# Performance work log

Hardware: AMD Instinct MI355X
Metric: run time of the kernel (lower is better)

The kernel has to match this reference:

```python
import jax, jax.numpy as jnp
import numpy as np

B, S, E = 2, 2048, 4096
H, KV, D = 32, 8, 128  # heads, kv heads, head_dim
ROPE_BASE = 500000.0


def setup_inputs() -> dict:
    key = jax.random.key(0)
    ks = jax.random.split(key, 5)
    scale = 0.02
    return {
        "x": jax.random.normal(ks[0], (B, S, E), dtype=jnp.float32),
        "wq": jax.random.normal(ks[1], (E, E), dtype=jnp.float32) * scale,
        "wk": jax.random.normal(ks[2], (KV * D, E), dtype=jnp.float32) * scale,
        "wv": jax.random.normal(ks[3], (KV * D, E), dtype=jnp.float32) * scale,
        "wo": jax.random.normal(ks[4], (E, E), dtype=jnp.float32) * scale,
        "input_pos": jnp.arange(S, dtype=jnp.int64 if jax.config.jax_enable_x64 else jnp.int32),
    }


def _rope(xh, input_pos):
    # xh: [B, H, S, D]; standard llama rotate-half RoPE
    half = D // 2
    inv_freq = 1.0 / (ROPE_BASE ** (jnp.arange(0, half, dtype=jnp.float32) / half))
    ang = input_pos.astype(jnp.float32)[:, None] * inv_freq[None, :]  # [S, half]
    cos, sin = jnp.cos(ang), jnp.sin(ang)
    x1, x2 = xh[..., :half], xh[..., half:]
    return jnp.concatenate([x1 * cos - x2 * sin, x2 * cos + x1 * sin], axis=-1)


def reference(x, wq, wk, wv, wo, input_pos):
    bsz, seq_len, _ = x.shape
    q = (x @ wq.T).reshape(bsz, seq_len, H, D).transpose(0, 2, 1, 3)    # [B,H,S,D]
    k = (x @ wk.T).reshape(bsz, seq_len, KV, D).transpose(0, 2, 1, 3)   # [B,KV,S,D]
    v = (x @ wv.T).reshape(bsz, seq_len, KV, D).transpose(0, 2, 1, 3)
    # repeat_kv: B (H R) S D with R = H // KV
    rep = H // KV
    k = jnp.repeat(k, rep, axis=1)
    v = jnp.repeat(v, rep, axis=1)
    q = _rope(q, input_pos)
    k = _rope(k, input_pos)
    # causal SDPA
    scores = jnp.einsum("bhqd,bhkd->bhqk", q, k) / jnp.sqrt(jnp.float32(D))
    causal = jnp.tril(jnp.ones((seq_len, seq_len), dtype=bool))
    scores = jnp.where(causal, scores, jnp.finfo(scores.dtype).min)
    probs = jax.nn.softmax(scores, axis=-1)
    out = jnp.einsum("bhqk,bhkd->bhqd", probs, v)                       # [B,H,S,D]
    out = out.transpose(0, 2, 1, 3).reshape(bsz, seq_len, E)
    return out @ wo.T
```

## Files before the change

### kernel.cpp

```cpp
#include <hip/hip_runtime.h>

#define B_ 2
#define S_ 2048
#define E_ 4096
#define H_ 32
#define KV_ 8
#define D_ 128

typedef __bf16 v8bf __attribute__((ext_vector_type(8)));
typedef __bf16 v4bf __attribute__((ext_vector_type(4)));
typedef float  v4f  __attribute__((ext_vector_type(4)));

static __device__ __forceinline__ v4f mfma16(v8bf a, v8bf b, v4f c) {
    return __builtin_amdgcn_mfma_f32_16x16x32_bf16(a, b, c, 0, 0, 0);
}

static __device__ __forceinline__ void load_lds16(const void* g, void* l) {
    __builtin_amdgcn_global_load_lds(
        (const __attribute__((address_space(1))) void*)g,
        (__attribute__((address_space(3))) void*)l, 16, 0, 0);
}

__global__ __launch_bounds__(256) void cast_f32_to_bf16(
        const float4* __restrict__ in, v4bf* __restrict__ out, int n4) {
    int i = blockIdx.x * blockDim.x + threadIdx.x;
    if (i >= n4) return;
    float4 v = in[i];
    v4bf o;
    o[0] = (__bf16)v.x; o[1] = (__bf16)v.y; o[2] = (__bf16)v.z; o[3] = (__bf16)v.w;
    out[i] = o;
}

__global__ __launch_bounds__(256) void rope_inplace(
        __bf16* __restrict__ qk, const int* __restrict__ pos, int nh,
        int rowstride, float outscale) {
    int idx = blockIdx.x * blockDim.x + threadIdx.x;
    int d = idx & 63;
    int t = idx >> 6;
    int h = t % nh;
    int bs = t / nh;
    if (bs >= B_ * S_) return;
    int s = bs & (S_ - 1);
    float p = (float)pos[s];
    float inv = expf(-(float)d * (1.0f / 64.0f) * 13.122363377404329f);
    float ang = p * inv;
    float c = cosf(ang), sn = sinf(ang);
    size_t off = (size_t)bs * rowstride + (size_t)h * D_;
    float x1 = (float)qk[off + d];
    float x2 = (float)qk[off + d + 64];
    qk[off + d]      = (__bf16)((x1 * c - x2 * sn) * outscale);
    qk[off + d + 64] = (__bf16)((x2 * c + x1 * sn) * outscale);
}

template <int EPI>
__global__ __launch_bounds__(512, 2) void gemm_bt(
        const __bf16* __restrict__ A, const __bf16* __restrict__ Bm,
        void* __restrict__ Cv, void* __restrict__ Cv2, int M, int N, int K) {
    __shared__ __bf16 As[2][256 * 64];
    __shared__ __bf16 Bs[2][256 * 64];
    const int tid  = threadIdx.x;
    const int wave = tid >> 6;
    const int lane = tid & 63;
    const int l15  = lane & 15;
    const int quad = lane >> 4;

    const int nbx = N >> 8;
    const int nwg = (int)gridDim.x;
    const int swz = ((int)blockIdx.x & 7) * (nwg >> 3) + ((int)blockIdx.x >> 3);
    const int bm  = (swz / nbx) * 256;
    const int bn  = (swz % nbx) * 256;

    const int wr = wave >> 2;
    const int wc = wave & 3;

    v4f acc[8][4] = {};

    const int srow = wave * 8 + (lane >> 3);
    const int scc  = (lane & 7) ^ ((lane >> 3) & 7);

    auto stage = [&](int t, int buf) {
        const size_t k0 = (size_t)t * 64;
#pragma unroll
        for (int g = 0; g < 4; ++g) {
            load_lds16(A + (size_t)(bm + g * 64 + srow) * K + k0 + scc * 8,
                       (char*)&As[buf][0] + (size_t)g * 8192 + (size_t)wave * 1024);
            load_lds16(Bm + (size_t)(bn + g * 64 + srow) * K + k0 + scc * 8,
                       (char*)&Bs[buf][0] + (size_t)g * 8192 + (size_t)wave * 1024);
        }
    };

    stage(0, 0);

    const int nt = K >> 6;
    for (int t = 0; t < nt; ++t) {
        const int cur = t & 1;
        if (t + 1 < nt) {
            stage(t + 1, cur ^ 1);
            asm volatile("s_waitcnt vmcnt(8)" ::: "memory");
        } else {
            asm volatile("s_waitcnt vmcnt(0)" ::: "memory");
        }
        __builtin_amdgcn_s_barrier();
        __builtin_amdgcn_sched_barrier(0);

        const __bf16* Asc = &As[cur][0];
        const __bf16* Bsc = &Bs[cur][0];
        v8bf a[4][2], b[2][2];

        auto rdA = [&](int mh) {
#pragma unroll
            for (int i = 0; i < 4; ++i)
#pragma unroll
                for (int kk = 0; kk < 2; ++kk)
                    a[i][kk] = *(const v8bf*)&Asc[
                        (wr * 128 + mh * 64 + i * 16 + l15) * 64 +
                        (((kk * 4 + quad) ^ (l15 & 7)) * 8)];
        };
        auto rdB = [&](int nh) {
#pragma unroll
            for (int j = 0; j < 2; ++j)
#pragma unroll
                for (int kk = 0; kk < 2; ++kk)
                    b[j][kk] = *(const v8bf*)&Bsc[
                        (wc * 64 + nh * 32 + j * 16 + l15) * 64 +
                        (((kk * 4 + quad) ^ (l15 & 7)) * 8)];
        };
        auto domfma = [&](int mh, int nh) {
            __builtin_amdgcn_s_setprio(1);
#pragma unroll
            for (int kk = 0; kk < 2; ++kk)
#pragma unroll
                for (int i = 0; i < 4; ++i)
#pragma unroll
                    for (int j = 0; j < 2; ++j)
                        acc[mh * 4 + i][nh * 2 + j] =
                            mfma16(a[i][kk], b[j][kk], acc[mh * 4 + i][nh * 2 + j]);
            __builtin_amdgcn_s_setprio(0);
        };

        rdA(0); rdB(0);
        __builtin_amdgcn_s_barrier();
        domfma(0, 0);
        __builtin_amdgcn_s_barrier();
        __builtin_amdgcn_sched_barrier(0);
        rdB(1);
        __builtin_amdgcn_s_barrier();
        domfma(0, 1);
        __builtin_amdgcn_s_barrier();
        __builtin_amdgcn_sched_barrier(0);
        rdA(1);
        __builtin_amdgcn_s_barrier();
        domfma(1, 1);
        __builtin_amdgcn_s_barrier();
        __builtin_amdgcn_sched_barrier(0);
        rdB(0);
        __builtin_amdgcn_s_barrier();
        domfma(1, 0);
        __builtin_amdgcn_s_barrier();
        __builtin_amdgcn_sched_barrier(0);
    }

#pragma unroll
    for (int mi = 0; mi < 8; ++mi) {
#pragma unroll
        for (int nj = 0; nj < 4; ++nj) {
#pragma unroll
            for (int r = 0; r < 4; ++r) {
                int row = bm + wr * 128 + mi * 16 + quad * 4 + r;
                int col = bn + wc * 64 + nj * 16 + l15;
                float val = acc[mi][nj][r];
                if (EPI == 0) {
                    ((float*)Cv)[(size_t)row * N + col] = val;
                } else if (EPI == 1) {
                    ((__bf16*)Cv)[(size_t)row * N + col] = (__bf16)val;
                } else {
                    if (col < 1024) {
                        ((__bf16*)Cv)[(size_t)row * 1024 + col] = (__bf16)val;
                    } else {
                        int cc = col - 1024;
                        int b  = row >> 11, s = row & (S_ - 1);
                        int kv = cc >> 7,  d = cc & (D_ - 1);
                        ((__bf16*)Cv2)[((size_t)((b * KV_ + kv) * D_ + d)) * S_ + s] = (__bf16)val;
                    }
                }
            }
        }
    }
}

__global__ __launch_bounds__(256, 2) void attn_fused(
        const __bf16* __restrict__ q, const __bf16* __restrict__ k,
        const __bf16* __restrict__ vt, __bf16* __restrict__ attn) {
    __shared__ __bf16 Ks[2][64 * 128];
    __shared__ __bf16 Vs[2][128 * 64];
    __shared__ __bf16 P[4][16 * 64];
    const int wave = threadIdx.x >> 6;
    const int lane = threadIdx.x & 63;

    const int wgid = blockIdx.x;
    const int xcd  = wgid & 7;
    const int slot = wgid >> 3;
    const int bh   = xcd * 8 + (slot >> 5);
    const int qblk = 31 - (slot & 31);
    const int b = bh >> 5;
    const int h = bh & 31;
    const int kvh = h >> 2;
    const int q0 = qblk * 64 + wave * 16;
    const int l15  = lane & 15;
    const int quad = lane >> 4;

    const __bf16* qbase = q  + (size_t)(b * S_) * E_ + (size_t)h * D_;
    const __bf16* kbase = k  + (size_t)(b * S_) * (KV_ * D_) + (size_t)kvh * D_;
    const __bf16* vbase = vt + (size_t)((b * KV_ + kvh) * D_) * S_;
    __bf16* Pw = &P[wave][0];

    const int krow_l = lane >> 4;
    const int kcc    = lane & 15;
    const int vrow_l = lane >> 3;
    const int vcc    = lane & 7;

    auto stageK = [&](int t, int buf) {
#pragma unroll
        for (int i = 0; i < 4; ++i) {
            int g = wave * 4 + i;
            int row = g * 4 + krow_l;
            int scc = kcc ^ (row & 15);
            load_lds16(kbase + (size_t)(t * 64 + row) * (KV_ * D_) + scc * 8,
                       (char*)&Ks[buf][0] + (size_t)g * 1024);
        }
    };
    auto stageV = [&](int t, int buf) {
#pragma unroll
        for (int i = 0; i < 4; ++i) {
            int g = wave * 4 + i;
            int row = g * 8 + vrow_l;
            int scc = vcc ^ (row & 7);
            load_lds16(vbase + (size_t)row * S_ + t * 64 + scc * 8,
                       (char*)&Vs[buf][0] + (size_t)g * 1024);
        }
    };

    stageK(0, 0);
    stageV(0, 0);

    v8bf aq[4];
#pragma unroll
    for (int kc = 0; kc < 4; ++kc)
        aq[kc] = *(const v8bf*)(qbase + (size_t)(q0 + l15) * E_ + kc * 32 + quad * 8);

    v4f o[8] = {};
    float m_i = -INFINITY, l_i = 0.f;

    const int ntiles = qblk + 1;

    for (int t = 0; t < ntiles; ++t) {
        const int cur = t & 1;
        if (t + 1 < ntiles) {
            stageK(t + 1, cur ^ 1);
            stageV(t + 1, cur ^ 1);
            asm volatile("s_waitcnt vmcnt(8)" ::: "memory");
        } else {
            asm volatile("s_waitcnt vmcnt(0)" ::: "memory");
        }
        __builtin_amdgcn_s_barrier();
        __builtin_amdgcn_sched_barrier(0);

        const int n0 = t * 64;
        const __bf16* Ksc = &Ks[cur][0];
        const __bf16* Vsc = &Vs[cur][0];

        v4f s[4] = {};
        __builtin_amdgcn_s_setprio(1);
#pragma unroll
        for (int kc = 0; kc < 4; ++kc) {
            v8bf kf[4];
#pragma unroll
            for (int j = 0; j < 4; ++j)
                kf[j] = *(const v8bf*)&Ksc[(j * 16 + l15) * 128 +
                                           (((kc * 4 + quad) ^ l15) * 8)];
#pragma unroll
            for (int j = 0; j < 4; ++j)
                s[j] = mfma16(kf[j], aq[kc], s[j]);
        }
        __builtin_amdgcn_s_setprio(0);

        float e[4][4];
        if (n0 + 63 > q0) {
#pragma unroll
            for (int j = 0; j < 4; ++j)
#pragma unroll
                for (int r = 0; r < 4; ++r) {
                    float v = s[j][r];
                    if (n0 + j * 16 + quad * 4 + r > q0 + l15) v = -INFINITY;
                    e[j][r] = v;
                }
        } else {
#pragma unroll
            for (int j = 0; j < 4; ++j)
#pragma unroll
                for (int r = 0; r < 4; ++r)
                    e[j][r] = s[j][r];
        }

        float mloc = e[0][0];
#pragma unroll
        for (int j = 0; j < 4; ++j)
#pragma unroll
            for (int r = 0; r < 4; ++r)
                mloc = fmaxf(mloc, e[j][r]);
        mloc = fmaxf(mloc, __shfl_xor(mloc, 16, 64));
        mloc = fmaxf(mloc, __shfl_xor(mloc, 32, 64));

        if (!__all(mloc - m_i <= 8.0f)) {
            float mnew = fmaxf(m_i, mloc);
            float alpha = __expf(m_i - mnew);
            m_i = mnew;
            l_i *= alpha;
            float af[4];
#pragma unroll
            for (int r = 0; r < 4; ++r)
                af[r] = __shfl(alpha, quad * 4 + r, 16);
#pragma unroll
            for (int c = 0; c < 8; ++c)
#pragma unroll
                for (int r = 0; r < 4; ++r)
                    o[c][r] *= af[r];
        }

        float psum = 0.f;
#pragma unroll
        for (int j = 0; j < 4; ++j)
#pragma unroll
            for (int r = 0; r < 4; ++r) {
                e[j][r] = __expf(e[j][r] - m_i);
                psum += e[j][r];
            }
        psum += __shfl_xor(psum, 16, 64);
        psum += __shfl_xor(psum, 32, 64);
        l_i += psum;

#pragma unroll
        for (int j = 0; j < 4; ++j) {
            v4bf pk;
#pragma unroll
            for (int r = 0; r < 4; ++r) pk[r] = (__bf16)e[j][r];
            int cl = j * 2 + (quad >> 1);
            *(v4bf*)&Pw[l15 * 64 + ((cl ^ (l15 & 7)) << 3) + ((quad & 1) << 2)] = pk;
        }

        v8bf ap0 = *(const v8bf*)&Pw[l15 * 64 + ((quad ^ (l15 & 7)) << 3)];
        v8bf ap1 = *(const v8bf*)&Pw[l15 * 64 + (((4 + quad) ^ (l15 & 7)) << 3)];

        __builtin_amdgcn_s_setprio(1);
#pragma unroll
        for (int c = 0; c < 8; ++c) {
            v8bf v0 = *(const v8bf*)&Vsc[(c * 16 + l15) * 64 +
                                         ((quad ^ (l15 & 7)) * 8)];
            v8bf v1 = *(const v8bf*)&Vsc[(c * 16 + l15) * 64 +
                                         (((4 + quad) ^ (l15 & 7)) * 8)];
            o[c] = mfma16(ap0, v0, o[c]);
            o[c] = mfma16(ap1, v1, o[c]);
        }
        __builtin_amdgcn_s_setprio(0);

        __builtin_amdgcn_sched_barrier(0);
        asm volatile("s_waitcnt lgkmcnt(0)" ::: "memory");
        __builtin_amdgcn_s_barrier();
        __builtin_amdgcn_sched_barrier(0);
    }

    float linv = 1.0f / l_i;
    float lr[4];
#pragma unroll
    for (int r = 0; r < 4; ++r)
        lr[r] = __shfl(linv, quad * 4 + r, 16);
    __bf16* obase = attn + (size_t)(b * S_) * E_ + (size_t)h * D_;
#pragma unroll
    for (int c = 0; c < 8; ++c)
#pragma unroll
        for (int r = 0; r < 4; ++r)
            obase[(size_t)(q0 + quad * 4 + r) * E_ + c * 16 + l15] =
                (__bf16)(o[c][r] * lr[r]);
}

extern "C" void kernel_launch(void* const* d_in, const int* in_sizes, int n_in,
                              void* d_out, int out_size, void* d_ws, size_t ws_size,
                              hipStream_t stream) {
    (void)in_sizes; (void)n_in; (void)out_size; (void)ws_size;
    const float* x  = (const float*)d_in[0];
    const float* wq = (const float*)d_in[1];
    const float* wk = (const float*)d_in[2];
    const float* wv = (const float*)d_in[3];
    const float* wo = (const float*)d_in[4];
    const int*   pos = (const int*)d_in[5];
    float* out = (float*)d_out;

    char* ws = (char*)d_ws;
    size_t off = 0;
    auto alloc = [&](size_t bytes) {
        char* p = ws + off;
        off += (bytes + 255) & ~(size_t)255;
        return p;
    };
    __bf16* xb   = (__bf16*)alloc((size_t)B_ * S_ * E_ * 2);
    __bf16* wqb  = (__bf16*)alloc((size_t)E_ * E_ * 2);
    __bf16* wkvb = (__bf16*)alloc((size_t)2 * KV_ * D_ * E_ * 2);
    __bf16* wob  = (__bf16*)alloc((size_t)E_ * E_ * 2);
    __bf16* qb   = (__bf16*)alloc((size_t)B_ * S_ * E_ * 2);
    __bf16* kb   = (__bf16*)alloc((size_t)B_ * S_ * KV_ * D_ * 2);
    __bf16* vt   = (__bf16*)alloc((size_t)B_ * KV_ * D_ * S_ * 2);
    __bf16* at   = (__bf16*)alloc((size_t)B_ * S_ * E_ * 2);

    auto cast = [&](const float* in, __bf16* ob, size_t n) {
        int n4 = (int)(n / 4);
        cast_f32_to_bf16<<<(n4 + 255) / 256, 256, 0, stream>>>(
            (const float4*)in, (v4bf*)ob, n4);
    };
    cast(x,  xb,  (size_t)B_ * S_ * E_);
    cast(wq, wqb, (size_t)E_ * E_);
    cast(wk, wkvb, (size_t)KV_ * D_ * E_);
    cast(wv, wkvb + (size_t)KV_ * D_ * E_, (size_t)KV_ * D_ * E_);
    cast(wo, wob, (size_t)E_ * E_);

    const int M = B_ * S_;
    const int nwg_e = (E_ / 256) * (M / 256);
    const int nwg_kv = (2 * KV_ * D_ / 256) * (M / 256);
    gemm_bt<1><<<dim3(nwg_e), 512, 0, stream>>>(
        xb, wqb, qb, nullptr, M, E_, E_);
    gemm_bt<2><<<dim3(nwg_kv), 512, 0, stream>>>(
        xb, wkvb, kb, vt, M, 2 * KV_ * D_, E_);

    rope_inplace<<<(B_ * S_ * H_ * 64 + 255) / 256, 256, 0, stream>>>(
        qb, pos, H_, E_, 0.08838834764831845f);
    rope_inplace<<<(B_ * S_ * KV_ * 64 + 255) / 256, 256, 0, stream>>>(
        kb, pos, KV_, KV_ * D_, 1.0f);

    attn_fused<<<dim3(B_ * H_ * (S_ / 64)), 256, 0, stream>>>(qb, kb, vt, at);

    gemm_bt<0><<<dim3(nwg_e), 512, 0, stream>>>(
        at, wob, out, nullptr, M, E_, E_);
}
```

Measured before the change: 889.1 us.

## Remove per-quadrant barriers in GEMM inner loop and keep both B halves in registers

Replaces the four read/barrier/MFMA phases per K-tile with one larger phase. Both B halves are held in registers (b0, b1), so the second rdB(0) reload is gone. The intra-tile s_barrier calls that kept waves in lockstep are removed, leaving one lgkmcnt wait and one barrier at the end of each tile. This cuts synchronisation and redundant LDS reads, but raises register pressure and gives up the explicit wave interleaving that let MFMA overlap LDS traffic across waves.

```diff
diff --git a/kernel.cpp b/kernel.cpp
--- a/kernel.cpp
+++ b/kernel.cpp
@@ -105,57 +105,71 @@
 
         const __bf16* Asc = &As[cur][0];
         const __bf16* Bsc = &Bs[cur][0];
-        v8bf a[4][2], b[2][2];
-
-        auto rdA = [&](int mh) {
+        v8bf a[4][2], b0[2][2], b1[2][2];
+
+#pragma unroll
+        for (int i = 0; i < 4; ++i)
+#pragma unroll
+            for (int kk = 0; kk < 2; ++kk)
+                a[i][kk] = *(const v8bf*)&Asc[
+                    (wr * 128 + i * 16 + l15) * 64 +
+                    (((kk * 4 + quad) ^ (l15 & 7)) * 8)];
+#pragma unroll
+        for (int j = 0; j < 2; ++j)
+#pragma unroll
+            for (int kk = 0; kk < 2; ++kk) {
+                b0[j][kk] = *(const v8bf*)&Bsc[
+                    (wc * 64 + j * 16 + l15) * 64 +
+                    (((kk * 4 + quad) ^ (l15 & 7)) * 8)];
+                b1[j][kk] = *(const v8bf*)&Bsc[
+                    (wc * 64 + 32 + j * 16 + l15) * 64 +
+                    (((kk * 4 + quad) ^ (l15 & 7)) * 8)];
+            }
+
+        __builtin_amdgcn_s_setprio(1);
+#pragma unroll
+        for (int kk = 0; kk < 2; ++kk)
 #pragma unroll
             for (int i = 0; i < 4; ++i)
 #pragma unroll
-                for (int kk = 0; kk < 2; ++kk)
-                    a[i][kk] = *(const v8bf*)&Asc[
-                        (wr * 128 + mh * 64 + i * 16 + l15) * 64 +
-                        (((kk * 4 + quad) ^ (l15 & 7)) * 8)];
-        };
-        auto rdB = [&](int nh) {
-#pragma unroll
-            for (int j = 0; j < 2; ++j)
-#pragma unroll
-                for (int kk = 0; kk < 2; ++kk)
-                    b[j][kk] = *(const v8bf*)&Bsc[
-                        (wc * 64 + nh * 32 + j * 16 + l15) * 64 +
-                        (((kk * 4 + quad) ^ (l15 & 7)) * 8)];
-        };
-        auto domfma = [&](int mh, int nh) {
-            __builtin_amdgcn_s_setprio(1);
+                for (int j = 0; j < 2; ++j)
+                    acc[i][j] = mfma16(a[i][kk], b0[j][kk], acc[i][j]);
+#pragma unroll
+        for (int kk = 0; kk < 2; ++kk)
+#pragma unroll
+            for (int i = 0; i < 4; ++i)
+#pragma unroll
+                for (int j = 0; j < 2; ++j)
+                    acc[i][2 + j] = mfma16(a[i][kk], b1[j][kk], acc[i][2 + j]);
+        __builtin_amdgcn_s_setprio(0);
+
+#pragma unroll
+        for (int i = 0; i < 4; ++i)
 #pragma unroll
             for (int kk = 0; kk < 2; ++kk)
-#pragma unroll
-                for (int i = 0; i < 4; ++i)
-#pragma unroll
-                    for (int j = 0; j < 2; ++j)
-                        acc[mh * 4 + i][nh * 2 + j] =
-                            mfma16(a[i][kk], b[j][kk], acc[mh * 4 + i][nh * 2 + j]);
-            __builtin_amdgcn_s_setprio(0);
-        };
-
-        rdA(0); rdB(0);
-        __builtin_amdgcn_s_barrier();
-        domfma(0, 0);
-        __builtin_amdgcn_s_barrier();
-        __builtin_amdgcn_sched_barrier(0);
-        rdB(1);
-        __builtin_amdgcn_s_barrier();
-        domfma(0, 1);
-        __builtin_amdgcn_s_barrier();
-        __builtin_amdgcn_sched_barrier(0);
-        rdA(1);
-        __builtin_amdgcn_s_barrier();
-        domfma(1, 1);
-        __builtin_amdgcn_s_barrier();
-        __builtin_amdgcn_sched_barrier(0);
-        rdB(0);
-        __builtin_amdgcn_s_barrier();
-        domfma(1, 0);
+                a[i][kk] = *(const v8bf*)&Asc[
+                    (wr * 128 + 64 + i * 16 + l15) * 64 +
+                    (((kk * 4 + quad) ^ (l15 & 7)) * 8)];
+
+        __builtin_amdgcn_s_setprio(1);
+#pragma unroll
+        for (int kk = 0; kk < 2; ++kk)
+#pragma unroll
+            for (int i = 0; i < 4; ++i)
+#pragma unroll
+                for (int j = 0; j < 2; ++j)
+                    acc[4 + i][2 + j] = mfma16(a[i][kk], b1[j][kk], acc[4 + i][2 + j]);
+#pragma unroll
+        for (int kk = 0; kk < 2; ++kk)
+#pragma unroll
+            for (int i = 0; i < 4; ++i)
+#pragma unroll
+                for (int j = 0; j < 2; ++j)
+                    acc[4 + i][j] = mfma16(a[i][kk], b0[j][kk], acc[4 + i][j]);
+        __builtin_amdgcn_s_setprio(0);
+
+        __builtin_amdgcn_sched_barrier(0);
+        asm volatile("s_waitcnt lgkmcnt(0)" ::: "memory");
         __builtin_amdgcn_s_barrier();
         __builtin_amdgcn_sched_barrier(0);
     }
```

After: 816.1 us. 8.2% less time.

## Fuse Q/KV projection GEMMs and pipeline quarter-tile LDS loads

Applied to the files above, without the earlier changes.

Merges the Q and KV projection GEMMs into one 384-workgroup launch, so the small KV GEMM no longer runs alone with poor occupancy and one launch is removed. The GEMM main loop now splits the LDS tile into four quarter buffers (A-top, B-left, B-right, A-bottom). It issues each quarter's next-k load right after that quarter is read, overlapping global-to-LDS transfers with MFMA phases. This adds finer vmcnt/barrier bookkeeping and more barriers per iteration, which could cost synchronization overhead.

```diff
diff --git a/kernel.cpp b/kernel.cpp
--- a/kernel.cpp
+++ b/kernel.cpp
@@ -52,17 +52,191 @@
     qk[off + d + 64] = (__bf16)((x2 * c + x1 * sn) * outscale);
 }
 
-template <int EPI>
-__global__ __launch_bounds__(512, 2) void gemm_bt(
-        const __bf16* __restrict__ A, const __bf16* __restrict__ Bm,
-        void* __restrict__ Cv, void* __restrict__ Cv2, int M, int N, int K) {
-    __shared__ __bf16 As[2][256 * 64];
-    __shared__ __bf16 Bs[2][256 * 64];
+#define GEMM_BODY(A_, Bm_, bm_, bn_, K_, H_ls, acc_)                           \
+    {                                                                          \
+        const int srow8 = tid >> 3;                                            \
+        const int scc   = (tid & 7) ^ (srow8 & 7);                             \
+        auto stageHT = [&](int t, int hh) {                                    \
+            char* dbase = (char*)&H_ls[t & 1][hh][0] + (size_t)wave * 1024;    \
+            const size_t kof = (size_t)t * 64 + scc * 8;                       \
+            if (hh == 0 || hh == 3) {                                          \
+                const int mh = (hh == 3);                                      \
+                _Pragma("unroll")                                              \
+                for (int g = 0; g < 2; ++g) {                                  \
+                    int row = bm_ + g * 128 + mh * 64 + srow8;                 \
+                    load_lds16(A_ + (size_t)row * K_ + kof, dbase + g * 8192); \
+                }                                                              \
+            } else {                                                           \
+                const int nh = (hh == 2);                                      \
+                _Pragma("unroll")                                              \
+                for (int g = 0; g < 2; ++g) {                                  \
+                    int sc  = g * 64 + srow8;                                  \
+                    int col = bn_ + (sc >> 5) * 64 + nh * 32 + (sc & 31);      \
+                    load_lds16(Bm_ + (size_t)col * K_ + kof, dbase + g * 8192);\
+                }                                                              \
+            }                                                                  \
+        };                                                                     \
+        stageHT(0, 0); stageHT(0, 1); stageHT(0, 2); stageHT(0, 3);            \
+        asm volatile("s_waitcnt vmcnt(4)" ::: "memory");                       \
+        __builtin_amdgcn_s_barrier();                                          \
+        const int nt = K_ >> 6;                                                \
+        for (int t = 0; t < nt; ++t) {                                         \
+            const int cur = t & 1;                                             \
+            const bool more = (t + 1 < nt);                                    \
+            const __bf16* A0p = &H_ls[cur][0][0];                              \
+            const __bf16* B0p = &H_ls[cur][1][0];                              \
+            const __bf16* B1p = &H_ls[cur][2][0];                              \
+            const __bf16* A1p = &H_ls[cur][3][0];                              \
+            v8bf a[4][2], b0[2][2], b1[2][2];                                  \
+            _Pragma("unroll")                                                  \
+            for (int i = 0; i < 4; ++i)                                        \
+                _Pragma("unroll")                                              \
+                for (int kk = 0; kk < 2; ++kk)                                 \
+                    a[i][kk] = *(const v8bf*)&A0p[(wr * 64 + i * 16 + l15) * 64\
+                        + (((kk * 4 + quad) ^ (l15 & 7)) * 8)];                \
+            _Pragma("unroll")                                                  \
+            for (int j = 0; j < 2; ++j)                                        \
+                _Pragma("unroll")                                              \
+                for (int kk = 0; kk < 2; ++kk)                                 \
+                    b0[j][kk] = *(const v8bf*)&B0p[(wc * 32 + j * 16 + l15) *  \
+                        64 + (((kk * 4 + quad) ^ (l15 & 7)) * 8)];             \
+            if (more) stageHT(t + 1, 0);                                       \
+            __builtin_amdgcn_s_barrier();                                      \
+            asm volatile("s_waitcnt lgkmcnt(0)" ::: "memory");                 \
+            __builtin_amdgcn_s_setprio(1);                                     \
+            _Pragma("unroll")                                                  \
+            for (int kk = 0; kk < 2; ++kk)                                     \
+                _Pragma("unroll")                                              \
+                for (int i = 0; i < 4; ++i)                                    \
+                    _Pragma("unroll")                                          \
+                    for (int j = 0; j < 2; ++j)                                \
+                        acc_[i][j] = mfma16(a[i][kk], b0[j][kk], acc_[i][j]);  \
+            __builtin_amdgcn_s_setprio(0);                                     \
+            if (more) asm volatile("s_waitcnt vmcnt(4)" ::: "memory");         \
+            else      asm volatile("s_waitcnt vmcnt(2)" ::: "memory");         \
+            __builtin_amdgcn_s_barrier();                                      \
+            _Pragma("unroll")                                                  \
+            for (int j = 0; j < 2; ++j)                                        \
+                _Pragma("unroll")                                              \
+                for (int kk = 0; kk < 2; ++kk)                                 \
+                    b1[j][kk] = *(const v8bf*)&B1p[(wc * 32 + j * 16 + l15) *  \
+                        64 + (((kk * 4 + quad) ^ (l15 & 7)) * 8)];             \
+            if (more) stageHT(t + 1, 1);                                       \
+            __builtin_amdgcn_s_barrier();                                      \
+            asm volatile("s_waitcnt lgkmcnt(0)" ::: "memory");                 \
+            __builtin_amdgcn_s_setprio(1);                                     \
+            _Pragma("unroll")                                                  \
+            for (int kk = 0; kk < 2; ++kk)                                     \
+                _Pragma("unroll")                                              \
+                for (int i = 0; i < 4; ++i)                                    \
+                    _Pragma("unroll")                                          \
+                    for (int j = 0; j < 2; ++j)                                \
+                        acc_[i][2 + j] =                                       \
+                            mfma16(a[i][kk], b1[j][kk], acc_[i][2 + j]);       \
+            __builtin_amdgcn_s_setprio(0);                                     \
+            if (more) asm volatile("s_waitcnt vmcnt(4)" ::: "memory");         \
+            else      asm volatile("s_waitcnt vmcnt(0)" ::: "memory");         \
+            __builtin_amdgcn_s_barrier();                                      \
+            _Pragma("unroll")                                                  \
+            for (int i = 0; i < 4; ++i)                                        \
+                _Pragma("unroll")                                              \
+                for (int kk = 0; kk < 2; ++kk)                                 \
+                    a[i][kk] = *(const v8bf*)&A1p[(wr * 64 + i * 16 + l15) * 64\
+                        + (((kk * 4 + quad) ^ (l15 & 7)) * 8)];                \
+            if (more) stageHT(t + 1, 2);                                       \
+            __builtin_amdgcn_s_barrier();                                      \
+            asm volatile("s_waitcnt lgkmcnt(0)" ::: "memory");                 \
+            __builtin_amdgcn_s_setprio(1);                                     \
+            _Pragma("unroll")                                                  \
+            for (int kk = 0; kk < 2; ++kk)                                     \
+                _Pragma("unroll")                                              \
+                for (int i = 0; i < 4; ++i)                                    \
+                    _Pragma("unroll")                                          \
+                    for (int j = 0; j < 2; ++j)                                \
+                        acc_[4 + i][2 + j] =                                   \
+                            mfma16(a[i][kk], b1[j][kk], acc_[4 + i][2 + j]);   \
+            __builtin_amdgcn_s_setprio(0);                                     \
+            __builtin_amdgcn_s_barrier();                                      \
+            if (more) stageHT(t + 1, 3);                                       \
+            __builtin_amdgcn_s_barrier();                                      \
+            __builtin_amdgcn_s_setprio(1);                                     \
+            _Pragma("unroll")                                                  \
+            for (int kk = 0; kk < 2; ++kk)                                     \
+                _Pragma("unroll")                                              \
+                for (int i = 0; i < 4; ++i)                                    \
+                    _Pragma("unroll")                                          \
+                    for (int j = 0; j < 2; ++j)                                \
+                        acc_[4 + i][j] =                                       \
+                            mfma16(a[i][kk], b0[j][kk], acc_[4 + i][j]);       \
+            __builtin_amdgcn_s_setprio(0);                                     \
+            if (more) asm volatile("s_waitcnt vmcnt(4)" ::: "memory");         \
+            __builtin_amdgcn_s_barrier();                                      \
+        }                                                                      \
+    }
+
+__global__ __launch_bounds__(512, 2) void gemm_qkv(
+        const __bf16* __restrict__ A, const __bf16* __restrict__ Wq,
+        const __bf16* __restrict__ Wkv, __bf16* __restrict__ Cq,
+        __bf16* __restrict__ Ck, __bf16* __restrict__ Cvt, int M, int K) {
+    __shared__ __bf16 H[2][4][128 * 64];
     const int tid  = threadIdx.x;
     const int wave = tid >> 6;
     const int lane = tid & 63;
     const int l15  = lane & 15;
     const int quad = lane >> 4;
+    const int wr = wave >> 2;
+    const int wc = wave & 3;
+
+    const int nwg = (int)gridDim.x;
+    const int swz = ((int)blockIdx.x & 7) * (nwg >> 3) + ((int)blockIdx.x >> 3);
+
+    const bool isQ = (swz < 256);
+    const int  id  = isQ ? swz : (swz - 256);
+    const int  nbx = isQ ? 16 : 8;
+    const int  bm  = (id / nbx) * 256;
+    const int  bn  = (id % nbx) * 256;
+    const __bf16* Bm = isQ ? Wq : Wkv;
+
+    v4f acc[8][4] = {};
+    GEMM_BODY(A, Bm, bm, bn, K, H, acc)
+
+#pragma unroll
+    for (int mi = 0; mi < 8; ++mi) {
+#pragma unroll
+        for (int nj = 0; nj < 4; ++nj) {
+#pragma unroll
+            for (int r = 0; r < 4; ++r) {
+                int row = bm + wr * 128 + mi * 16 + quad * 4 + r;
+                int col = bn + wc * 64 + nj * 16 + l15;
+                float val = acc[mi][nj][r];
+                if (isQ) {
+                    Cq[(size_t)row * E_ + col] = (__bf16)val;
+                } else {
+                    if (col < 1024) {
+                        Ck[(size_t)row * 1024 + col] = (__bf16)val;
+                    } else {
+                        int cc = col - 1024;
+                        int b  = row >> 11, s = row & (S_ - 1);
+                        int kv = cc >> 7,  d = cc & (D_ - 1);
+                        Cvt[((size_t)((b * KV_ + kv) * D_ + d)) * S_ + s] = (__bf16)val;
+                    }
+                }
+            }
+        }
+    }
+}
+
+__global__ __launch_bounds__(512, 2) void gemm_out(
+        const __bf16* __restrict__ A, const __bf16* __restrict__ Bm,
+        float* __restrict__ C, int M, int N, int K) {
+    __shared__ __bf16 H[2][4][128 * 64];
+    const int tid  = threadIdx.x;
+    const int wave = tid >> 6;
+    const int lane = tid & 63;
+    const int l15  = lane & 15;
+    const int quad = lane >> 4;
+    const int wr = wave >> 2;
+    const int wc = wave & 3;
 
     const int nbx = N >> 8;
     const int nwg = (int)gridDim.x;
@@ -70,122 +244,19 @@
     const int bm  = (swz / nbx) * 256;
     const int bn  = (swz % nbx) * 256;
 
-    const int wr = wave >> 2;
-    const int wc = wave & 3;
-
     v4f acc[8][4] = {};
-
-    const int srow = wave * 8 + (lane >> 3);
-    const int scc  = (lane & 7) ^ ((lane >> 3) & 7);
-
-    auto stage = [&](int t, int buf) {
-        const size_t k0 = (size_t)t * 64;
-#pragma unroll
-        for (int g = 0; g < 4; ++g) {
-            load_lds16(A + (size_t)(bm + g * 64 + srow) * K + k0 + scc * 8,
-                       (char*)&As[buf][0] + (size_t)g * 8192 + (size_t)wave * 1024);
-            load_lds16(Bm + (size_t)(bn + g * 64 + srow) * K + k0 + scc * 8,
-                       (char*)&Bs[buf][0] + (size_t)g * 8192 + (size_t)wave * 1024);
-        }
-    };
-
-    stage(0, 0);
-
-    const int nt = K >> 6;
-    for (int t = 0; t < nt; ++t) {
-        const int cur = t & 1;
-        if (t + 1 < nt) {
-            stage(t + 1, cur ^ 1);
-            asm volatile("s_waitcnt vmcnt(8)" ::: "memory");
-        } else {
-            asm volatile("s_waitcnt vmcnt(0)" ::: "memory");
-        }
-        __builtin_amdgcn_s_barrier();
-        __builtin_amdgcn_sched_barrier(0);
-
-        const __bf16* Asc = &As[cur][0];
-        const __bf16* Bsc = &Bs[cur][0];
-        v8bf a[4][2], b[2][2];
-
-        auto rdA = [&](int mh) {
-#pragma unroll
-            for (int i = 0; i < 4; ++i)
-#pragma unroll
-                for (int kk = 0; kk < 2; ++kk)
-                    a[i][kk] = *(const v8bf*)&Asc[
-                        (wr * 128 + mh * 64 + i * 16 + l15) * 64 +
-                        (((kk * 4 + quad) ^ (l15 & 7)) * 8)];
-        };
-        auto rdB = [&](int nh) {
-#pragma unroll
-            for (int j = 0; j < 2; ++j)
-#pragma unroll
-                for (int kk = 0; kk < 2; ++kk)
-                    b[j][kk] = *(const v8bf*)&Bsc[
-                        (wc * 64 + nh * 32 + j * 16 + l15) * 64 +
-                        (((kk * 4 + quad) ^ (l15 & 7)) * 8)];
-        };
-        auto domfma = [&](int mh, int nh) {
-            __builtin_amdgcn_s_setprio(1);
-#pragma unroll
-            for (int kk = 0; kk < 2; ++kk)
-#pragma unroll
-                for (int i = 0; i < 4; ++i)
-#pragma unroll
-                    for (int j = 0; j < 2; ++j)
-                        acc[mh * 4 + i][nh * 2 + j] =
-                            mfma16(a[i][kk], b[j][kk], acc[mh * 4 + i][nh * 2 + j]);
-            __builtin_amdgcn_s_setprio(0);
-        };
-
-        rdA(0); rdB(0);
-        __builtin_amdgcn_s_barrier();
-        domfma(0, 0);
-        __builtin_amdgcn_s_barrier();
-        __builtin_amdgcn_sched_barrier(0);
-        rdB(1);
-        __builtin_amdgcn_s_barrier();
-        domfma(0, 1);
-        __builtin_amdgcn_s_barrier();
-        __builtin_amdgcn_sched_barrier(0);
-        rdA(1);
-        __builtin_amdgcn_s_barrier();
-        domfma(1, 1);
-        __builtin_amdgcn_s_barrier();
-        __builtin_amdgcn_sched_barrier(0);
-        rdB(0);
-        __builtin_amdgcn_s_barrier();
-        domfma(1, 0);
-        __builtin_amdgcn_s_barrier();
-        __builtin_amdgcn_sched_barrier(0);
-    }
-
-#pragma unroll
-    for (int mi = 0; mi < 8; ++mi) {
-#pragma unroll
-        for (int nj = 0; nj < 4; ++nj) {
+    GEMM_BODY(A, Bm, bm, bn, K, H, acc)
+
+#pragma unroll
+    for (int mi = 0; mi < 8; ++mi)
+#pragma unroll
+        for (int nj = 0; nj < 4; ++nj)
 #pragma unroll
             for (int r = 0; r < 4; ++r) {
                 int row = bm + wr * 128 + mi * 16 + quad * 4 + r;
                 int col = bn + wc * 64 + nj * 16 + l15;
-                float val = acc[mi][nj][r];
-                if (EPI == 0) {
-                    ((float*)Cv)[(size_t)row * N + col] = val;
-                } else if (EPI == 1) {
-                    ((__bf16*)Cv)[(size_t)row * N + col] = (__bf16)val;
-                } else {
-                    if (col < 1024) {
-                        ((__bf16*)Cv)[(size_t)row * 1024 + col] = (__bf16)val;
-                    } else {
-                        int cc = col - 1024;
-                        int b  = row >> 11, s = row & (S_ - 1);
-                        int kv = cc >> 7,  d = cc & (D_ - 1);
-                        ((__bf16*)Cv2)[((size_t)((b * KV_ + kv) * D_ + d)) * S_ + s] = (__bf16)val;
-                    }
-                }
+                C[(size_t)row * N + col] = acc[mi][nj][r];
             }
-        }
-    }
 }
 
 __global__ __launch_bounds__(256, 2) void attn_fused(
@@ -423,12 +494,8 @@
     cast(wo, wob, (size_t)E_ * E_);
 
     const int M = B_ * S_;
-    const int nwg_e = (E_ / 256) * (M / 256);
-    const int nwg_kv = (2 * KV_ * D_ / 256) * (M / 256);
-    gemm_bt<1><<<dim3(nwg_e), 512, 0, stream>>>(
-        xb, wqb, qb, nullptr, M, E_, E_);
-    gemm_bt<2><<<dim3(nwg_kv), 512, 0, stream>>>(
-        xb, wkvb, kb, vt, M, 2 * KV_ * D_, E_);
+    gemm_qkv<<<dim3(384), 512, 0, stream>>>(
+        xb, wqb, wkvb, qb, kb, vt, M, E_);
 
     rope_inplace<<<(B_ * S_ * H_ * 64 + 255) / 256, 256, 0, stream>>>(
         qb, pos, H_, E_, 0.08838834764831845f);
@@ -437,6 +504,6 @@
 
     attn_fused<<<dim3(B_ * H_ * (S_ / 64)), 256, 0, stream>>>(qb, kb, vt, at);
 
-    gemm_bt<0><<<dim3(nwg_e), 512, 0, stream>>>(
-        at, wob, out, nullptr, M, E_, E_);
-}
+    gemm_out<<<dim3((E_ / 256) * (M / 256)), 512, 0, stream>>>(
+        at, wob, out, M, E_, E_);
+}
```

Result: faster. 768.1 us (-13.6%).
